# Kernel tuning notes

Hardware: AMD Instinct MI355X
Metric: run time of the kernel (lower is better)

The kernel has to match this reference:

```python
import jax, jax.numpy as jnp
import numpy as np

WIRES = 4
N_LAYERS = 2
NUM_CLASSES = 10


def _apply_ry(state, c, s, axis):
    # state: [N,2,2,2,2]; apply Ry with cos/sin halves c,s on given qubit axis.
    st = jnp.moveaxis(state, axis, -1)
    a0, a1 = st[..., 0], st[..., 1]
    st = jnp.stack([c * a0 - s * a1, s * a0 + c * a1], axis=-1)
    return jnp.moveaxis(st, -1, axis)


def _cnot(state, ctrl, tgt):
    st = jnp.moveaxis(state, (ctrl, tgt), (-2, -1))
    st = jnp.stack([st[..., 0, :], st[..., 1, ::-1]], axis=-2)
    return jnp.moveaxis(st, (-2, -1), (ctrl, tgt))


def _simulate(angles, params):
    # angles: [N,4] encoding Ry angles; params: [L,4]. Returns PauliZ expvals [N,4].
    N = angles.shape[0]
    state = jnp.zeros((N, 2, 2, 2, 2), dtype=angles.dtype).at[:, 0, 0, 0, 0].set(1.0)
    half = angles * 0.5
    for i in range(WIRES):
        c = jnp.cos(half[:, i])[:, None, None, None]
        s = jnp.sin(half[:, i])[:, None, None, None]
        state = _apply_ry(state, c, s, 1 + i)
    for l in range(params.shape[0]):
        for i in range(WIRES):
            th = params[l, i] * 0.5
            state = _apply_ry(state, jnp.cos(th), jnp.sin(th), 1 + i)
        for i in range(WIRES - 1):
            state = _cnot(state, 1 + i, 2 + i)
        state = _cnot(state, WIRES, 1)  # CNOT(last, 0)
    probs = state ** 2
    sign = jnp.array([1.0, -1.0], dtype=angles.dtype)
    zs = [jnp.einsum('nabcd,' + 'abcd'[i] + '->n', probs, sign) for i in range(WIRES)]
    return jnp.stack(zs, axis=1)


def setup_inputs() -> dict:
    key = jax.random.key(0)
    k1, k2, k3, k4 = jax.random.split(key, 4)
    B = 8192
    x = jax.random.uniform(k1, (B, 28, 28), dtype=jnp.float32)
    params = jax.random.normal(k2, (N_LAYERS, WIRES), dtype=jnp.float32)
    W = jax.random.normal(k3, (NUM_CLASSES, WIRES * 14 * 14), dtype=jnp.float32) * 0.02
    b = jnp.zeros((NUM_CLASSES,), dtype=jnp.float32)
    return {"x": x, "params": params, "W": W, "b": b}


def reference(x, params, W, b):
    B = x.shape[0]
    # Extract 2x2 patches in row-major order: [B,196,4] matching torch loop.
    angles = x.reshape(B, 14, 2, 14, 2).transpose(0, 1, 3, 2, 4).reshape(B * 196, 4)
    feats = _simulate(angles, params).reshape(B, 196 * WIRES)  # [B,784]
    logits = feats @ W.T + b
    return jax.nn.log_softmax(logits, axis=-1)
```

## Files before the change

### kernel.cpp

```cpp
#include <hip/hip_runtime.h>


template <int BIT>
static __device__ __forceinline__ void apply_ry_tan(float (&a)[16], float t) {
#pragma unroll
    for (int i = 0; i < 16; ++i) {
        if (i & (1 << BIT)) continue;
        float a0 = a[i];
        float a1 = a[i | (1 << BIT)];
        a[i]              = fmaf(-t, a1, a0);
        a[i | (1 << BIT)] = fmaf( t, a0, a1);
    }
}

template <int CBIT, int TBIT>
static __device__ __forceinline__ void apply_cnot(float (&a)[16]) {
#pragma unroll
    for (int i = 0; i < 16; ++i) {
        if ((i & (1 << CBIT)) && !(i & (1 << TBIT))) {
            float t = a[i];
            a[i] = a[i | (1 << TBIT)];
            a[i | (1 << TBIT)] = t;
        }
    }
}

__global__ __launch_bounds__(256) void quanv_fused_kernel(
    const float* __restrict__ x,
    const float* __restrict__ params,
    const float* __restrict__ W,
    const float* __restrict__ bias,
    float* __restrict__ out,
    int B)
{
    __shared__ float Wl[10 * 784];

    {
        const float4* Wg4 = (const float4*)W;
        float4* Wl4 = (float4*)Wl;
#pragma unroll
        for (int t = threadIdx.x; t < 1960; t += 256) Wl4[t] = Wg4[t];
    }
    __syncthreads();

    const int lane = threadIdx.x & 63;
    const int lid  = lane & 31;
    const int wave = threadIdx.x >> 6;
    const int row  = blockIdx.x * 8 + wave * 2 + (lane >> 5);
    if (row >= B) return;

    float h0[4], t1w[4];
    float scale2 = 1.0f;
#pragma unroll
    for (int w = 0; w < 4; ++w) {
        h0[w] = 0.5f * params[w];
        float s, c;
        __sincosf(0.5f * params[4 + w], &s, &c);
        t1w[w] = s / c;
        scale2 *= c;
    }
    scale2 *= scale2;

    float logit[10];
#pragma unroll
    for (int c = 0; c < 10; ++c) logit[c] = 0.0f;

    const float* xrow = x + (size_t)row * 784;

#pragma unroll 1
    for (int p = lid; p < 196; p += 32) {
        const int i = p / 14;
        const int j = p - i * 14;

        const float* b0 = xrow + i * 56 + j * 2;
        float2 r0 = *(const float2*)b0;
        float2 r1 = *(const float2*)(b0 + 28);

        float c0, s0, c1, s1, c2, s2, c3, s3;
        __sincosf(fmaf(0.5f, r0.x, h0[0]), &s0, &c0);
        __sincosf(fmaf(0.5f, r0.y, h0[1]), &s1, &c1);
        __sincosf(fmaf(0.5f, r1.x, h0[2]), &s2, &c2);
        __sincosf(fmaf(0.5f, r1.y, h0[3]), &s3, &c3);

        float p01[4] = {c0 * c1, c0 * s1, s0 * c1, s0 * s1};
        float p23[4] = {c2 * c3, c2 * s3, s2 * c3, s2 * s3};
        float amp[16];
#pragma unroll
        for (int idx = 0; idx < 16; ++idx)
            amp[idx] = p01[idx >> 2] * p23[idx & 3];

        apply_cnot<3, 2>(amp);
        apply_cnot<2, 1>(amp);
        apply_cnot<1, 0>(amp);
        apply_cnot<0, 3>(amp);
        apply_ry_tan<3>(amp, t1w[0]);
        apply_ry_tan<2>(amp, t1w[1]);
        apply_ry_tan<1>(amp, t1w[2]);
        apply_ry_tan<0>(amp, t1w[3]);
        apply_cnot<3, 2>(amp);
        apply_cnot<2, 1>(amp);
        apply_cnot<1, 0>(amp);
        apply_cnot<0, 3>(amp);

        float pr[16];
#pragma unroll
        for (int idx = 0; idx < 16; ++idx) pr[idx] = amp[idx] * amp[idx];

        float sp[8], dp[8];
#pragma unroll
        for (int k = 0; k < 8; ++k) {
            sp[k] = pr[2 * k] + pr[2 * k + 1];
            dp[k] = pr[2 * k] - pr[2 * k + 1];
        }
        float z3 = ((dp[0] + dp[1]) + (dp[2] + dp[3])) + ((dp[4] + dp[5]) + (dp[6] + dp[7]));
        float t[4], u[4];
#pragma unroll
        for (int k = 0; k < 4; ++k) {
            t[k] = sp[2 * k] + sp[2 * k + 1];
            u[k] = sp[2 * k] - sp[2 * k + 1];
        }
        float z2 = (u[0] + u[1]) + (u[2] + u[3]);
        float z1 = (t[0] - t[1]) + (t[2] - t[3]);
        float z0 = (t[0] + t[1]) - (t[2] + t[3]);

        const float* wp = Wl + 4 * p;
#pragma unroll
        for (int c = 0; c < 10; ++c) {
            float4 wv = *(const float4*)(wp + c * 784);
            logit[c] = fmaf(z0, wv.x, fmaf(z1, wv.y, fmaf(z2, wv.z, fmaf(z3, wv.w, logit[c]))));
        }
    }

#pragma unroll
    for (int off = 16; off > 0; off >>= 1) {
#pragma unroll
        for (int c = 0; c < 10; ++c)
            logit[c] += __shfl_xor(logit[c], off, 64);
    }

    if (lid == 0) {
        float v[10];
        float m = -1e30f;
#pragma unroll
        for (int c = 0; c < 10; ++c) {
            v[c] = fmaf(scale2, logit[c], bias[c]);
            m = fmaxf(m, v[c]);
        }
        float sum = 0.f;
#pragma unroll
        for (int c = 0; c < 10; ++c) sum += __expf(v[c] - m);
        float lse = m + __logf(sum);

        float2* o = (float2*)(out + (size_t)row * 10);
#pragma unroll
        for (int k = 0; k < 5; ++k)
            o[k] = make_float2(v[2 * k] - lse, v[2 * k + 1] - lse);
    }
}

extern "C" void kernel_launch(void* const* d_in, const int* in_sizes, int n_in,
                              void* d_out, int out_size, void* d_ws, size_t ws_size,
                              hipStream_t stream) {
    const float* x      = (const float*)d_in[0];
    const float* params = (const float*)d_in[1];
    const float* W      = (const float*)d_in[2];
    const float* bias   = (const float*)d_in[3];
    float* out          = (float*)d_out;

    const int B = in_sizes[0] / 784;
    const int blocks = (B + 7) / 8;

    hipLaunchKernelGGL(quanv_fused_kernel, dim3(blocks), dim3(256), 0, stream,
                       x, params, W, bias, out, B);
}
```

Measured before the change: 83.24 us.

## Process two rows per half-wave with software-prefetched patch loads

Each 32-lane half-wave now handles two batch rows, so every shared-memory W load feeds two sets of logit FMAs, and the block count is halved. The next iteration's patch pixels are loaded before the current patch is simulated, to hide global-load latency. Launch bounds gain a min-blocks hint of 2. This raises register pressure (two logit arrays, two simulations in flight) and halves the number of blocks, and rowB is not bounds-checked for odd B.

```diff
diff --git a/kernel.cpp b/kernel.cpp
--- a/kernel.cpp
+++ b/kernel.cpp
@@ -25,7 +25,58 @@
     }
 }
 
-__global__ __launch_bounds__(256) void quanv_fused_kernel(
+static __device__ __forceinline__ void sim_patch(
+    float2 r0, float2 r1, const float (&h0)[4], const float (&t1w)[4], float (&z)[4])
+{
+    float c0, s0, c1, s1, c2, s2, c3, s3;
+    __sincosf(fmaf(0.5f, r0.x, h0[0]), &s0, &c0);
+    __sincosf(fmaf(0.5f, r0.y, h0[1]), &s1, &c1);
+    __sincosf(fmaf(0.5f, r1.x, h0[2]), &s2, &c2);
+    __sincosf(fmaf(0.5f, r1.y, h0[3]), &s3, &c3);
+
+    float p01[4] = {c0 * c1, c0 * s1, s0 * c1, s0 * s1};
+    float p23[4] = {c2 * c3, c2 * s3, s2 * c3, s2 * s3};
+    float amp[16];
+#pragma unroll
+    for (int idx = 0; idx < 16; ++idx)
+        amp[idx] = p01[idx >> 2] * p23[idx & 3];
+
+    apply_cnot<3, 2>(amp);
+    apply_cnot<2, 1>(amp);
+    apply_cnot<1, 0>(amp);
+    apply_cnot<0, 3>(amp);
+    apply_ry_tan<3>(amp, t1w[0]);
+    apply_ry_tan<2>(amp, t1w[1]);
+    apply_ry_tan<1>(amp, t1w[2]);
+    apply_ry_tan<0>(amp, t1w[3]);
+    apply_cnot<3, 2>(amp);
+    apply_cnot<2, 1>(amp);
+    apply_cnot<1, 0>(amp);
+    apply_cnot<0, 3>(amp);
+
+    float pr[16];
+#pragma unroll
+    for (int idx = 0; idx < 16; ++idx) pr[idx] = amp[idx] * amp[idx];
+
+    float sp[8], dp[8];
+#pragma unroll
+    for (int k = 0; k < 8; ++k) {
+        sp[k] = pr[2 * k] + pr[2 * k + 1];
+        dp[k] = pr[2 * k] - pr[2 * k + 1];
+    }
+    z[3] = ((dp[0] + dp[1]) + (dp[2] + dp[3])) + ((dp[4] + dp[5]) + (dp[6] + dp[7]));
+    float t[4], u[4];
+#pragma unroll
+    for (int k = 0; k < 4; ++k) {
+        t[k] = sp[2 * k] + sp[2 * k + 1];
+        u[k] = sp[2 * k] - sp[2 * k + 1];
+    }
+    z[2] = (u[0] + u[1]) + (u[2] + u[3]);
+    z[1] = (t[0] - t[1]) + (t[2] - t[3]);
+    z[0] = (t[0] + t[1]) - (t[2] + t[3]);
+}
+
+__global__ __launch_bounds__(256, 2) void quanv_fused_kernel(
     const float* __restrict__ x,
     const float* __restrict__ params,
     const float* __restrict__ W,
@@ -46,8 +97,9 @@
     const int lane = threadIdx.x & 63;
     const int lid  = lane & 31;
     const int wave = threadIdx.x >> 6;
-    const int row  = blockIdx.x * 8 + wave * 2 + (lane >> 5);
-    if (row >= B) return;
+    const int rowA = blockIdx.x * 16 + wave * 4 + (lane >> 5) * 2;
+    if (rowA >= B) return;
+    const int rowB = rowA + 1;
 
     float h0[4], t1w[4];
     float scale2 = 1.0f;
@@ -61,100 +113,89 @@
     }
     scale2 *= scale2;
 
-    float logit[10];
-#pragma unroll
-    for (int c = 0; c < 10; ++c) logit[c] = 0.0f;
-
-    const float* xrow = x + (size_t)row * 784;
+    float logitA[10], logitB[10];
+#pragma unroll
+    for (int c = 0; c < 10; ++c) { logitA[c] = 0.0f; logitB[c] = 0.0f; }
+
+    const float* xA = x + (size_t)rowA * 784;
+    const float* xB = x + (size_t)rowB * 784;
+
+    int p = lid;
+    int i = p / 14, j = p - i * 14;
+    int off = i * 56 + j * 2;
+    float2 a0 = *(const float2*)(xA + off), a1 = *(const float2*)(xA + off + 28);
+    float2 b0 = *(const float2*)(xB + off), b1 = *(const float2*)(xB + off + 28);
 
 #pragma unroll 1
-    for (int p = lid; p < 196; p += 32) {
-        const int i = p / 14;
-        const int j = p - i * 14;
-
-        const float* b0 = xrow + i * 56 + j * 2;
-        float2 r0 = *(const float2*)b0;
-        float2 r1 = *(const float2*)(b0 + 28);
-
-        float c0, s0, c1, s1, c2, s2, c3, s3;
-        __sincosf(fmaf(0.5f, r0.x, h0[0]), &s0, &c0);
-        __sincosf(fmaf(0.5f, r0.y, h0[1]), &s1, &c1);
-        __sincosf(fmaf(0.5f, r1.x, h0[2]), &s2, &c2);
-        __sincosf(fmaf(0.5f, r1.y, h0[3]), &s3, &c3);
-
-        float p01[4] = {c0 * c1, c0 * s1, s0 * c1, s0 * s1};
-        float p23[4] = {c2 * c3, c2 * s3, s2 * c3, s2 * s3};
-        float amp[16];
-#pragma unroll
-        for (int idx = 0; idx < 16; ++idx)
-            amp[idx] = p01[idx >> 2] * p23[idx & 3];
-
-        apply_cnot<3, 2>(amp);
-        apply_cnot<2, 1>(amp);
-        apply_cnot<1, 0>(amp);
-        apply_cnot<0, 3>(amp);
-        apply_ry_tan<3>(amp, t1w[0]);
-        apply_ry_tan<2>(amp, t1w[1]);
-        apply_ry_tan<1>(amp, t1w[2]);
-        apply_ry_tan<0>(amp, t1w[3]);
-        apply_cnot<3, 2>(amp);
-        apply_cnot<2, 1>(amp);
-        apply_cnot<1, 0>(amp);
-        apply_cnot<0, 3>(amp);
-
-        float pr[16];
-#pragma unroll
-        for (int idx = 0; idx < 16; ++idx) pr[idx] = amp[idx] * amp[idx];
-
-        float sp[8], dp[8];
-#pragma unroll
-        for (int k = 0; k < 8; ++k) {
-            sp[k] = pr[2 * k] + pr[2 * k + 1];
-            dp[k] = pr[2 * k] - pr[2 * k + 1];
-        }
-        float z3 = ((dp[0] + dp[1]) + (dp[2] + dp[3])) + ((dp[4] + dp[5]) + (dp[6] + dp[7]));
-        float t[4], u[4];
-#pragma unroll
-        for (int k = 0; k < 4; ++k) {
-            t[k] = sp[2 * k] + sp[2 * k + 1];
-            u[k] = sp[2 * k] - sp[2 * k + 1];
-        }
-        float z2 = (u[0] + u[1]) + (u[2] + u[3]);
-        float z1 = (t[0] - t[1]) + (t[2] - t[3]);
-        float z0 = (t[0] + t[1]) - (t[2] + t[3]);
+    for (int k = 0; k < 6; ++k) {
+        const int pn = p + 32;
+        float2 na0, na1, nb0, nb1;
+        if (pn < 196) {
+            const int ni = pn / 14, nj = pn - ni * 14;
+            const int noff = ni * 56 + nj * 2;
+            na0 = *(const float2*)(xA + noff); na1 = *(const float2*)(xA + noff + 28);
+            nb0 = *(const float2*)(xB + noff); nb1 = *(const float2*)(xB + noff + 28);
+        }
+
+        float zA[4], zB[4];
+        sim_patch(a0, a1, h0, t1w, zA);
+        sim_patch(b0, b1, h0, t1w, zB);
 
         const float* wp = Wl + 4 * p;
 #pragma unroll
         for (int c = 0; c < 10; ++c) {
             float4 wv = *(const float4*)(wp + c * 784);
-            logit[c] = fmaf(z0, wv.x, fmaf(z1, wv.y, fmaf(z2, wv.z, fmaf(z3, wv.w, logit[c]))));
-        }
-    }
-
-#pragma unroll
-    for (int off = 16; off > 0; off >>= 1) {
-#pragma unroll
-        for (int c = 0; c < 10; ++c)
-            logit[c] += __shfl_xor(logit[c], off, 64);
+            logitA[c] = fmaf(zA[0], wv.x, fmaf(zA[1], wv.y, fmaf(zA[2], wv.z, fmaf(zA[3], wv.w, logitA[c]))));
+            logitB[c] = fmaf(zB[0], wv.x, fmaf(zB[1], wv.y, fmaf(zB[2], wv.z, fmaf(zB[3], wv.w, logitB[c]))));
+        }
+
+        p = pn;
+        a0 = na0; a1 = na1; b0 = nb0; b1 = nb1;
+    }
+
+    if (p < 196) {
+        float zA[4], zB[4];
+        sim_patch(a0, a1, h0, t1w, zA);
+        sim_patch(b0, b1, h0, t1w, zB);
+        const float* wp = Wl + 4 * p;
+#pragma unroll
+        for (int c = 0; c < 10; ++c) {
+            float4 wv = *(const float4*)(wp + c * 784);
+            logitA[c] = fmaf(zA[0], wv.x, fmaf(zA[1], wv.y, fmaf(zA[2], wv.z, fmaf(zA[3], wv.w, logitA[c]))));
+            logitB[c] = fmaf(zB[0], wv.x, fmaf(zB[1], wv.y, fmaf(zB[2], wv.z, fmaf(zB[3], wv.w, logitB[c]))));
+        }
+    }
+
+#pragma unroll
+    for (int o = 16; o > 0; o >>= 1) {
+#pragma unroll
+        for (int c = 0; c < 10; ++c) {
+            logitA[c] += __shfl_xor(logitA[c], o, 64);
+            logitB[c] += __shfl_xor(logitB[c], o, 64);
+        }
     }
 
     if (lid == 0) {
-        float v[10];
-        float m = -1e30f;
-#pragma unroll
-        for (int c = 0; c < 10; ++c) {
-            v[c] = fmaf(scale2, logit[c], bias[c]);
-            m = fmaxf(m, v[c]);
-        }
-        float sum = 0.f;
-#pragma unroll
-        for (int c = 0; c < 10; ++c) sum += __expf(v[c] - m);
-        float lse = m + __logf(sum);
-
-        float2* o = (float2*)(out + (size_t)row * 10);
-#pragma unroll
-        for (int k = 0; k < 5; ++k)
-            o[k] = make_float2(v[2 * k] - lse, v[2 * k + 1] - lse);
+#pragma unroll
+        for (int r = 0; r < 2; ++r) {
+            const float* lg = r ? logitB : logitA;
+            float v[10];
+            float m = -1e30f;
+#pragma unroll
+            for (int c = 0; c < 10; ++c) {
+                v[c] = fmaf(scale2, lg[c], bias[c]);
+                m = fmaxf(m, v[c]);
+            }
+            float sum = 0.f;
+#pragma unroll
+            for (int c = 0; c < 10; ++c) sum += __expf(v[c] - m);
+            float lse = m + __logf(sum);
+
+            float2* o2 = (float2*)(out + (size_t)(rowA + r) * 10);
+#pragma unroll
+            for (int k = 0; k < 5; ++k)
+                o2[k] = make_float2(v[2 * k] - lse, v[2 * k + 1] - lse);
+        }
     }
 }
 
@@ -168,7 +209,7 @@
     float* out          = (float*)d_out;
 
     const int B = in_sizes[0] / 784;
-    const int blocks = (B + 7) / 8;
+    const int blocks = (B + 15) / 16;
 
     hipLaunchKernelGGL(quanv_fused_kernel, dim3(blocks), dim3(256), 0, stream,
                        x, params, W, bias, out, B);
```

After: 84.95 us. +2.1%, slower.
